# Optimization experiments

Hardware: AMD Instinct MI355X
Metric: run time of the kernel (lower is better)

The kernel has to match this reference:

```python
import jax, jax.numpy as jnp
import numpy as np

N = 50000          # nodes
E = 800000         # edges (avg degree 16)
IN_C = 3
HEADS = 4
NUM_GRAPHS = 8
NUM_CLASSES = 10


def setup_inputs() -> dict:
    key = jax.random.key(0)
    ks = jax.random.split(key, 12)
    x = jax.random.normal(ks[0], (N, IN_C), jnp.float32)
    edge_index = jax.random.randint(ks[1], (2, E), 0, N, dtype=jnp.int64)
    batch = jnp.sort(jax.random.randint(ks[2], (N,), 0, NUM_GRAPHS, dtype=jnp.int64))

    def glorot(k, shape, fan):
        return jax.random.normal(k, shape, jnp.float32) * np.float32(1.0 / np.sqrt(fan))

    return {
        "x": x, "edge_index": edge_index, "batch": batch,
        "fc0_w": glorot(ks[3], (IN_C, 16), IN_C), "fc0_b": jnp.zeros((16,), jnp.float32),
        "u1": glorot(ks[4], (16, HEADS), 16), "c1": jnp.zeros((HEADS,), jnp.float32),
        "w1": glorot(ks[5], (16, HEADS * 32), 16), "b1": jnp.zeros((32,), jnp.float32),
        "u2": glorot(ks[6], (32, HEADS), 32), "c2": jnp.zeros((HEADS,), jnp.float32),
        "w2": glorot(ks[7], (32, HEADS * 64), 32), "b2": jnp.zeros((64,), jnp.float32),
        "fc1_w": glorot(ks[8], (64, NUM_CLASSES), 64), "fc1_b": jnp.zeros((NUM_CLASSES,), jnp.float32),
    }


def feast_conv(x, src, dst, u, c, w, b, heads, out_c):
    """FeaStConv (t_inv=True): per-edge head softmax on (x_j - x_i), mean aggregation."""
    n = x.shape[0]
    # soft-assignment over heads: [E, H]
    q = jax.nn.softmax((x[src] - x[dst]) @ u + c, axis=-1)
    # transform at node level, then gather per edge: [E, H, out_c]
    xw = (x @ w).reshape(n, heads, out_c)
    msg = jnp.einsum('eh,ehc->ec', q, xw[src])           # [E, out_c]
    agg = jax.ops.segment_sum(msg, dst, num_segments=n)  # sum over incoming edges
    cnt = jax.ops.segment_sum(jnp.ones((src.shape[0],), x.dtype), dst, num_segments=n)
    return agg / jnp.maximum(cnt, 1.0)[:, None] + b


def global_mean_pool(x, batch, num_graphs):
    s = jax.ops.segment_sum(x, batch, num_segments=num_graphs)
    cnt = jax.ops.segment_sum(jnp.ones((x.shape[0],), x.dtype), batch, num_segments=num_graphs)
    return s / jnp.maximum(cnt, 1.0)[:, None]


def reference(x, edge_index, batch, fc0_w, fc0_b, u1, c1, w1, b1, u2, c2, w2, b2, fc1_w, fc1_b):
    src, dst = edge_index[0], edge_index[1]   # x_j = x[src], x_i = x[dst]
    h = jax.nn.relu(x @ fc0_w + fc0_b)                              # [N, 16]
    h = jax.nn.relu(feast_conv(h, src, dst, u1, c1, w1, b1, HEADS, 32))  # [N, 32]
    h = jax.nn.relu(feast_conv(h, src, dst, u2, c2, w2, b2, HEADS, 64))  # [N, 64]
    g = global_mean_pool(h, batch, NUM_GRAPHS)                      # [G, 64]
    # dropout is identity in eval mode
    return g @ fc1_w + fc1_b                                        # [G, num_classes]
```

## Files before the change

kernel.cpp:

```cpp
#include <hip/hip_runtime.h>

#define N_NODES 50000
#define N_EDGES 800000
#define HEADS 4
#define NUM_GRAPHS 8

__global__ __launch_bounds__(256) void hist_kernel(const int* __restrict__ dst,
                                                   int* __restrict__ deg,
                                                   int* __restrict__ off) {
  int e = blockIdx.x * blockDim.x + threadIdx.x;
  if (e < N_EDGES) off[e] = atomicAdd(&deg[dst[e]], 1);
}

__global__ __launch_bounds__(256) void alloc_kernel(const int* __restrict__ deg,
                                                    int* __restrict__ gctr,
                                                    int* __restrict__ rowstart) {
  int i = blockIdx.x * blockDim.x + threadIdx.x;
  int lane = threadIdx.x & 63;
  int d = (i < N_NODES) ? deg[i] : 0;
  int pre = d;
#pragma unroll
  for (int offd = 1; offd < 64; offd <<= 1) {
    int v = __shfl_up(pre, offd, 64);
    if (lane >= offd) pre += v;
  }
  int total = __shfl(pre, 63, 64);
  int base = 0;
  if (lane == 63) base = atomicAdd(gctr, total);
  base = __shfl(base, 63, 64);
  if (i < N_NODES) rowstart[i] = base + pre - d;
}

__global__ __launch_bounds__(256) void scatter_kernel(const int* __restrict__ src,
                                                      const int* __restrict__ dst,
                                                      const int* __restrict__ rowstart,
                                                      const int* __restrict__ off,
                                                      int2* __restrict__ sd) {
  int e = blockIdx.x * blockDim.x + threadIdx.x;
  if (e >= N_EDGES) return;
  int d = dst[e];
  int p = rowstart[d] + off[e];
  sd[p] = make_int2(src[e], d);
}

__global__ __launch_bounds__(256) void fc0_kernel(
    const float* __restrict__ x,
    const float* __restrict__ fc0_w, const float* __restrict__ fc0_b,
    const float* __restrict__ u1,
    float* __restrict__ h0, float* __restrict__ P1) {
  __shared__ float sW0[3 * 16];
  __shared__ float sB0[16];
  __shared__ float sU[16 * 4];
  for (int i = threadIdx.x; i < 48; i += blockDim.x) sW0[i] = fc0_w[i];
  for (int i = threadIdx.x; i < 16; i += blockDim.x) sB0[i] = fc0_b[i];
  for (int i = threadIdx.x; i < 64; i += blockDim.x) sU[i] = u1[i];
  __syncthreads();
  int n = blockIdx.x * blockDim.x + threadIdx.x;
  if (n >= N_NODES) return;
  float x0 = x[n * 3 + 0], x1 = x[n * 3 + 1], x2 = x[n * 3 + 2];
  float h[16];
#pragma unroll
  for (int j = 0; j < 16; j++) {
    float v = x0 * sW0[0 * 16 + j] + x1 * sW0[1 * 16 + j] + x2 * sW0[2 * 16 + j] + sB0[j];
    h[j] = fmaxf(v, 0.f);
    h0[(size_t)n * 16 + j] = h[j];
  }
  float p0 = 0.f, p1 = 0.f, p2 = 0.f, p3 = 0.f;
#pragma unroll
  for (int j = 0; j < 16; j++) {
    p0 += h[j] * sU[j * 4 + 0];
    p1 += h[j] * sU[j * 4 + 1];
    p2 += h[j] * sU[j * 4 + 2];
    p3 += h[j] * sU[j * 4 + 3];
  }
  reinterpret_cast<float4*>(P1)[n] = make_float4(p0, p1, p2, p3);
}

__global__ __launch_bounds__(256) void q_kernel(
    const int2* __restrict__ sd,
    const float* __restrict__ P, const float* __restrict__ cb,
    float* __restrict__ q_perm) {
  int p = blockIdx.x * blockDim.x + threadIdx.x;
  if (p >= N_EDGES) return;
  int2 e = sd[p];
  float4 Ps = reinterpret_cast<const float4*>(P)[e.x];
  float4 Pd = reinterpret_cast<const float4*>(P)[e.y];
  float l0 = Ps.x - Pd.x + cb[0];
  float l1 = Ps.y - Pd.y + cb[1];
  float l2 = Ps.z - Pd.z + cb[2];
  float l3 = Ps.w - Pd.w + cb[3];
  float m = fmaxf(fmaxf(l0, l1), fmaxf(l2, l3));
  float e0v = __expf(l0 - m), e1v = __expf(l1 - m), e2v = __expf(l2 - m), e3v = __expf(l3 - m);
  float inv = 1.f / (e0v + e1v + e2v + e3v);
  reinterpret_cast<float4*>(q_perm)[p] =
      make_float4(e0v * inv, e1v * inv, e2v * inv, e3v * inv);
}

__global__ __launch_bounds__(256) void agg1_kernel(
    const int* __restrict__ rowstart, const int* __restrict__ deg,
    const int2* __restrict__ sd, const float* __restrict__ q_perm,
    const float* __restrict__ h0,
    float* __restrict__ A) {
  int wave = threadIdx.x >> 6;
  int lane = threadIdx.x & 63;
  int g = lane >> 4;
  int j = lane & 15;
  int node = blockIdx.x * 4 + wave;
  if (node >= N_NODES) return;
  int e0 = rowstart[node];
  int e1 = e0 + deg[node];
  const float4* q4 = reinterpret_cast<const float4*>(q_perm);
  float a0 = 0.f, a1 = 0.f, a2 = 0.f, a3 = 0.f;
  int p = e0;
  for (; p + 16 <= e1; p += 16) {
    int sA = sd[p + 0 + g].x;
    int sB = sd[p + 4 + g].x;
    int sC = sd[p + 8 + g].x;
    int sD = sd[p + 12 + g].x;
    float4 qA = q4[p + 0 + g];
    float4 qB = q4[p + 4 + g];
    float4 qC = q4[p + 8 + g];
    float4 qD = q4[p + 12 + g];
    float fA = h0[(size_t)sA * 16 + j];
    float fB = h0[(size_t)sB * 16 + j];
    float fC = h0[(size_t)sC * 16 + j];
    float fD = h0[(size_t)sD * 16 + j];
    a0 += qA.x * fA + qB.x * fB + qC.x * fC + qD.x * fD;
    a1 += qA.y * fA + qB.y * fB + qC.y * fC + qD.y * fD;
    a2 += qA.z * fA + qB.z * fB + qC.z * fC + qD.z * fD;
    a3 += qA.w * fA + qB.w * fB + qC.w * fC + qD.w * fD;
  }
  for (; p + 4 <= e1; p += 4) {
    int s = sd[p + g].x;
    float4 q = q4[p + g];
    float f = h0[(size_t)s * 16 + j];
    a0 += q.x * f; a1 += q.y * f; a2 += q.z * f; a3 += q.w * f;
  }
  int rem = e1 - p;
  if (g < rem) {
    int s = sd[p + g].x;
    float4 q = q4[p + g];
    float f = h0[(size_t)s * 16 + j];
    a0 += q.x * f; a1 += q.y * f; a2 += q.z * f; a3 += q.w * f;
  }
  a0 += __shfl_xor(a0, 16, 64); a0 += __shfl_xor(a0, 32, 64);
  a1 += __shfl_xor(a1, 16, 64); a1 += __shfl_xor(a1, 32, 64);
  a2 += __shfl_xor(a2, 16, 64); a2 += __shfl_xor(a2, 32, 64);
  a3 += __shfl_xor(a3, 16, 64); a3 += __shfl_xor(a3, 32, 64);
  float o = (g == 0) ? a0 : (g == 1) ? a1 : (g == 2) ? a2 : a3;
  A[(size_t)node * 64 + lane] = o;
}

__global__ __launch_bounds__(256) void agg2_kernel(
    const int* __restrict__ rowstart, const int* __restrict__ deg,
    const int2* __restrict__ sd, const float* __restrict__ q_perm,
    const float* __restrict__ h1,
    float* __restrict__ A) {
  int wave = threadIdx.x >> 6;
  int lane = threadIdx.x & 63;
  int g = lane >> 5;
  int j = lane & 31;
  int node = blockIdx.x * 4 + wave;
  if (node >= N_NODES) return;
  int e0 = rowstart[node];
  int e1 = e0 + deg[node];
  const float4* q4 = reinterpret_cast<const float4*>(q_perm);
  float a0 = 0.f, a1 = 0.f, a2 = 0.f, a3 = 0.f;
  int p = e0;
  for (; p + 8 <= e1; p += 8) {
    int sA = sd[p + 0 + g].x;
    int sB = sd[p + 2 + g].x;
    int sC = sd[p + 4 + g].x;
    int sD = sd[p + 6 + g].x;
    float4 qA = q4[p + 0 + g];
    float4 qB = q4[p + 2 + g];
    float4 qC = q4[p + 4 + g];
    float4 qD = q4[p + 6 + g];
    float fA = h1[(size_t)sA * 32 + j];
    float fB = h1[(size_t)sB * 32 + j];
    float fC = h1[(size_t)sC * 32 + j];
    float fD = h1[(size_t)sD * 32 + j];
    a0 += qA.x * fA + qB.x * fB + qC.x * fC + qD.x * fD;
    a1 += qA.y * fA + qB.y * fB + qC.y * fC + qD.y * fD;
    a2 += qA.z * fA + qB.z * fB + qC.z * fC + qD.z * fD;
    a3 += qA.w * fA + qB.w * fB + qC.w * fC + qD.w * fD;
  }
  for (; p + 2 <= e1; p += 2) {
    int s = sd[p + g].x;
    float4 q = q4[p + g];
    float f = h1[(size_t)s * 32 + j];
    a0 += q.x * f; a1 += q.y * f; a2 += q.z * f; a3 += q.w * f;
  }
  int rem = e1 - p;
  if (g < rem) {
    int s = sd[p + g].x;
    float4 q = q4[p + g];
    float f = h1[(size_t)s * 32 + j];
    a0 += q.x * f; a1 += q.y * f; a2 += q.z * f; a3 += q.w * f;
  }
  a0 += __shfl_xor(a0, 32, 64);
  a1 += __shfl_xor(a1, 32, 64);
  a2 += __shfl_xor(a2, 32, 64);
  a3 += __shfl_xor(a3, 32, 64);
  float oa = (g == 0) ? a0 : a1;
  float ob = (g == 0) ? a2 : a3;
  A[(size_t)node * 128 + lane] = oa;
  A[(size_t)node * 128 + 64 + lane] = ob;
}

__global__ __launch_bounds__(256) void gemm1_kernel(
    const int* __restrict__ deg, const float* __restrict__ A,
    const float* __restrict__ w1, const float* __restrict__ b1,
    const float* __restrict__ u2,
    float* __restrict__ h1, float* __restrict__ P2) {
  __shared__ float sB[64 * 32];
  __shared__ float sU[32 * 4];
  for (int i = threadIdx.x; i < 64 * 32; i += 256) {
    int hj = i / 32, c = i % 32;
    sB[i] = w1[(hj % 16) * 128 + (hj / 16) * 32 + c];
  }
  for (int i = threadIdx.x; i < 128; i += 256) sU[i] = u2[i];
  __syncthreads();
  const float4* sB4 = reinterpret_cast<const float4*>(sB);
  int c4 = threadIdx.x & 7;
  int g = threadIdx.x >> 3;
  int n0 = blockIdx.x * 64 + g * 2;
  int n1 = n0 + 1;
  int na = min(n0, N_NODES - 1);
  int nb = min(n1, N_NODES - 1);
  const float4* A0 = reinterpret_cast<const float4*>(A + (size_t)na * 64);
  const float4* A1 = reinterpret_cast<const float4*>(A + (size_t)nb * 64);
  float4 bc = reinterpret_cast<const float4*>(b1)[c4];
  float4 acc0 = {0, 0, 0, 0}, acc1 = {0, 0, 0, 0};
#pragma unroll 2
  for (int k4 = 0; k4 < 16; k4++) {
    float4 a0 = A0[k4];
    float4 a1 = A1[k4];
    float4 w0 = sB4[(4 * k4 + 0) * 8 + c4];
    float4 wv1 = sB4[(4 * k4 + 1) * 8 + c4];
    float4 w2v = sB4[(4 * k4 + 2) * 8 + c4];
    float4 w3 = sB4[(4 * k4 + 3) * 8 + c4];
    acc0.x += a0.x * w0.x + a0.y * wv1.x + a0.z * w2v.x + a0.w * w3.x;
    acc0.y += a0.x * w0.y + a0.y * wv1.y + a0.z * w2v.y + a0.w * w3.y;
    acc0.z += a0.x * w0.z + a0.y * wv1.z + a0.z * w2v.z + a0.w * w3.z;
    acc0.w += a0.x * w0.w + a0.y * wv1.w + a0.z * w2v.w + a0.w * w3.w;
    acc1.x += a1.x * w0.x + a1.y * wv1.x + a1.z * w2v.x + a1.w * w3.x;
    acc1.y += a1.x * w0.y + a1.y * wv1.y + a1.z * w2v.y + a1.w * w3.y;
    acc1.z += a1.x * w0.z + a1.y * wv1.z + a1.z * w2v.z + a1.w * w3.z;
    acc1.w += a1.x * w0.w + a1.y * wv1.w + a1.z * w2v.w + a1.w * w3.w;
  }
  float inv0 = 1.f / fmaxf((float)deg[na], 1.f);
  float inv1 = 1.f / fmaxf((float)deg[nb], 1.f);
  float4 o0 = {fmaxf(acc0.x * inv0 + bc.x, 0.f), fmaxf(acc0.y * inv0 + bc.y, 0.f),
               fmaxf(acc0.z * inv0 + bc.z, 0.f), fmaxf(acc0.w * inv0 + bc.w, 0.f)};
  float4 o1 = {fmaxf(acc1.x * inv1 + bc.x, 0.f), fmaxf(acc1.y * inv1 + bc.y, 0.f),
               fmaxf(acc1.z * inv1 + bc.z, 0.f), fmaxf(acc1.w * inv1 + bc.w, 0.f)};
  if (n0 < N_NODES) reinterpret_cast<float4*>(h1 + (size_t)n0 * 32)[c4] = o0;
  if (n1 < N_NODES) reinterpret_cast<float4*>(h1 + (size_t)n1 * 32)[c4] = o1;
  float pa[4] = {0, 0, 0, 0}, pb[4] = {0, 0, 0, 0};
#pragma unroll
  for (int k = 0; k < 4; k++) {
    int c = 4 * c4 + k;
    float v0 = k == 0 ? o0.x : k == 1 ? o0.y : k == 2 ? o0.z : o0.w;
    float v1 = k == 0 ? o1.x : k == 1 ? o1.y : k == 2 ? o1.z : o1.w;
#pragma unroll
    for (int hh = 0; hh < 4; hh++) {
      pa[hh] += v0 * sU[c * 4 + hh];
      pb[hh] += v1 * sU[c * 4 + hh];
    }
  }
#pragma unroll
  for (int msk = 1; msk <= 4; msk <<= 1) {
#pragma unroll
    for (int hh = 0; hh < 4; hh++) {
      pa[hh] += __shfl_xor(pa[hh], msk, 64);
      pb[hh] += __shfl_xor(pb[hh], msk, 64);
    }
  }
  if (c4 == 0) {
    if (n0 < N_NODES)
      reinterpret_cast<float4*>(P2)[n0] = make_float4(pa[0], pa[1], pa[2], pa[3]);
    if (n1 < N_NODES)
      reinterpret_cast<float4*>(P2)[n1] = make_float4(pb[0], pb[1], pb[2], pb[3]);
  }
}

__global__ __launch_bounds__(256) void gemm2_kernel(
    const int* __restrict__ deg, const float* __restrict__ A,
    const float* __restrict__ w2, const float* __restrict__ b2,
    float* __restrict__ h2) {
  __shared__ float sB[128 * 64];
  for (int i = threadIdx.x; i < 128 * 64; i += 256) {
    int hj = i / 64, c = i % 64;
    sB[i] = w2[(hj % 32) * 256 + (hj / 32) * 64 + c];
  }
  __syncthreads();
  const float4* sB4 = reinterpret_cast<const float4*>(sB);
  int c4 = threadIdx.x & 15;
  int g = threadIdx.x >> 4;
  int n0 = blockIdx.x * 32 + g * 2;
  int n1 = n0 + 1;
  int na = min(n0, N_NODES - 1);
  int nb = min(n1, N_NODES - 1);
  const float4* A0 = reinterpret_cast<const float4*>(A + (size_t)na * 128);
  const float4* A1 = reinterpret_cast<const float4*>(A + (size_t)nb * 128);
  float4 bc = reinterpret_cast<const float4*>(b2)[c4];
  float4 acc0 = {0, 0, 0, 0}, acc1 = {0, 0, 0, 0};
#pragma unroll 2
  for (int k4 = 0; k4 < 32; k4++) {
    float4 a0 = A0[k4];
    float4 a1 = A1[k4];
    float4 w0 = sB4[(4 * k4 + 0) * 16 + c4];
    float4 wv1 = sB4[(4 * k4 + 1) * 16 + c4];
    float4 w2v = sB4[(4 * k4 + 2) * 16 + c4];
    float4 w3 = sB4[(4 * k4 + 3) * 16 + c4];
    acc0.x += a0.x * w0.x + a0.y * wv1.x + a0.z * w2v.x + a0.w * w3.x;
    acc0.y += a0.x * w0.y + a0.y * wv1.y + a0.z * w2v.y + a0.w * w3.y;
    acc0.z += a0.x * w0.z + a0.y * wv1.z + a0.z * w2v.z + a0.w * w3.z;
    acc0.w += a0.x * w0.w + a0.y * wv1.w + a0.z * w2v.w + a0.w * w3.w;
    acc1.x += a1.x * w0.x + a1.y * wv1.x + a1.z * w2v.x + a1.w * w3.x;
    acc1.y += a1.x * w0.y + a1.y * wv1.y + a1.z * w2v.y + a1.w * w3.y;
    acc1.z += a1.x * w0.z + a1.y * wv1.z + a1.z * w2v.z + a1.w * w3.z;
    acc1.w += a1.x * w0.w + a1.y * wv1.w + a1.z * w2v.w + a1.w * w3.w;
  }
  if (n0 < N_NODES) {
    float inv = 1.f / fmaxf((float)deg[n0], 1.f);
    float4 o = {fmaxf(acc0.x * inv + bc.x, 0.f), fmaxf(acc0.y * inv + bc.y, 0.f),
                fmaxf(acc0.z * inv + bc.z, 0.f), fmaxf(acc0.w * inv + bc.w, 0.f)};
    reinterpret_cast<float4*>(h2 + (size_t)n0 * 64)[c4] = o;
  }
  if (n1 < N_NODES) {
    float inv = 1.f / fmaxf((float)deg[n1], 1.f);
    float4 o = {fmaxf(acc1.x * inv + bc.x, 0.f), fmaxf(acc1.y * inv + bc.y, 0.f),
                fmaxf(acc1.z * inv + bc.z, 0.f), fmaxf(acc1.w * inv + bc.w, 0.f)};
    reinterpret_cast<float4*>(h2 + (size_t)n1 * 64)[c4] = o;
  }
}

#define POOL_CHUNK 64
__global__ __launch_bounds__(256) void pool_kernel(
    const float* __restrict__ h2, const int* __restrict__ batch,
    float* __restrict__ gsum, float* __restrict__ gcnt) {
  int grp = threadIdx.x / 64;
  int c = threadIdx.x % 64;
  int n0 = (blockIdx.x * 4 + grp) * POOL_CHUNK;
  int n1 = min(n0 + POOL_CHUNK, N_NODES);
  if (n0 >= N_NODES) return;
  float acc = 0.f;
  float cacc = 0.f;
  int curg = batch[n0];
  for (int n = n0; n < n1; n++) {
    int g = batch[n];
    float v = h2[(size_t)n * 64 + c];
    if (g != curg) {
      atomicAdd(&gsum[curg * 64 + c], acc);
      if (c == 0) atomicAdd(&gcnt[curg], cacc);
      acc = 0.f;
      cacc = 0.f;
      curg = g;
    }
    acc += v;
    cacc += 1.f;
  }
  atomicAdd(&gsum[curg * 64 + c], acc);
  if (c == 0) atomicAdd(&gcnt[curg], cacc);
}

__global__ __launch_bounds__(128) void head_kernel(
    const float* __restrict__ gsum, const float* __restrict__ gcnt,
    const float* __restrict__ fc1_w, const float* __restrict__ fc1_b,
    float* __restrict__ out) {
  int t = threadIdx.x;
  if (t >= NUM_GRAPHS * 10) return;
  int g = t / 10, k = t % 10;
  float inv = 1.f / fmaxf(gcnt[g], 1.f);
  float s = fc1_b[k];
#pragma unroll
  for (int c = 0; c < 64; c++) s += gsum[g * 64 + c] * inv * fc1_w[c * 10 + k];
  out[g * 10 + k] = s;
}

extern "C" void kernel_launch(void* const* d_in, const int* in_sizes, int n_in,
                              void* d_out, int out_size, void* d_ws, size_t ws_size,
                              hipStream_t stream) {
  const float* x = (const float*)d_in[0];
  const int* edge_index = (const int*)d_in[1];
  const int* batch = (const int*)d_in[2];
  const float* fc0_w = (const float*)d_in[3];
  const float* fc0_b = (const float*)d_in[4];
  const float* u1 = (const float*)d_in[5];
  const float* c1 = (const float*)d_in[6];
  const float* w1 = (const float*)d_in[7];
  const float* b1 = (const float*)d_in[8];
  const float* u2 = (const float*)d_in[9];
  const float* c2 = (const float*)d_in[10];
  const float* w2 = (const float*)d_in[11];
  const float* b2 = (const float*)d_in[12];
  const float* fc1_w = (const float*)d_in[13];
  const float* fc1_b = (const float*)d_in[14];
  float* out = (float*)d_out;

  const int* src = edge_index;
  const int* dst = edge_index + N_EDGES;

  char* wsb = (char*)d_ws;
  int* deg = (int*)wsb;
  int* gctr = deg + N_NODES;
  float* gsum = (float*)wsb + 50004;
  float* gcnt = gsum + NUM_GRAPHS * 64;
  int* rowstart = (int*)wsb + 50524;
  int* off = rowstart + N_NODES;
  int2* sd = (int2*)((int*)wsb + 900524);
  float* q_perm = (float*)wsb + 2500524;
  float* h0 = q_perm + (size_t)N_EDGES * 4;
  float* h1 = h0 + (size_t)N_NODES * 16;
  float* h2 = h1 + (size_t)N_NODES * 32;
  float* A = h2 + (size_t)N_NODES * 64;
  float* P1 = A + (size_t)N_NODES * 128;
  float* P2 = P1 + (size_t)N_NODES * 4;

  hipMemsetAsync(d_ws, 0, 50524 * sizeof(int), stream);

  int nblk = (N_NODES + 255) / 256;
  int eblk = (N_EDGES + 255) / 256;
  int wblk = (N_NODES + 3) / 4;

  hist_kernel<<<eblk, 256, 0, stream>>>(dst, deg, off);
  alloc_kernel<<<nblk, 256, 0, stream>>>(deg, gctr, rowstart);
  scatter_kernel<<<eblk, 256, 0, stream>>>(src, dst, rowstart, off, sd);

  fc0_kernel<<<nblk, 256, 0, stream>>>(x, fc0_w, fc0_b, u1, h0, P1);

  q_kernel<<<eblk, 256, 0, stream>>>(sd, P1, c1, q_perm);
  agg1_kernel<<<wblk, 256, 0, stream>>>(rowstart, deg, sd, q_perm, h0, A);
  gemm1_kernel<<<(N_NODES + 63) / 64, 256, 0, stream>>>(deg, A, w1, b1, u2, h1, P2);

  q_kernel<<<eblk, 256, 0, stream>>>(sd, P2, c2, q_perm);
  agg2_kernel<<<wblk, 256, 0, stream>>>(rowstart, deg, sd, q_perm, h1, A);
  gemm2_kernel<<<(N_NODES + 31) / 32, 256, 0, stream>>>(deg, A, w2, b2, h2);

  int pblk = (N_NODES + POOL_CHUNK * 4 - 1) / (POOL_CHUNK * 4);
  pool_kernel<<<pblk, 256, 0, stream>>>(h2, batch, gsum, gcnt);
  head_kernel<<<1, 128, 0, stream>>>(gsum, gcnt, fc1_w, fc1_b, out);
}
```

Measured before the change: 281.7 us.

## Fuse edge softmax into aggregation kernels and merge histogram with fc0

After: 275.3 us, median of 3. 1.02x faster.

```diff
diff --git a/kernel.cpp b/kernel.cpp
--- a/kernel.cpp
+++ b/kernel.cpp
@@ -5,11 +5,46 @@
 #define HEADS 4
 #define NUM_GRAPHS 8
 
-__global__ __launch_bounds__(256) void hist_kernel(const int* __restrict__ dst,
-                                                   int* __restrict__ deg,
-                                                   int* __restrict__ off) {
-  int e = blockIdx.x * blockDim.x + threadIdx.x;
-  if (e < N_EDGES) off[e] = atomicAdd(&deg[dst[e]], 1);
+#define EBLK ((N_EDGES + 255) / 256)
+#define NBLK ((N_NODES + 255) / 256)
+
+__global__ __launch_bounds__(256) void hist_fc0_kernel(
+    const int* __restrict__ dst, int* __restrict__ deg, int* __restrict__ off,
+    const float* __restrict__ x,
+    const float* __restrict__ fc0_w, const float* __restrict__ fc0_b,
+    const float* __restrict__ u1,
+    float* __restrict__ h0, float* __restrict__ P1) {
+  if (blockIdx.x < EBLK) {
+    int e = blockIdx.x * 256 + threadIdx.x;
+    if (e < N_EDGES) off[e] = atomicAdd(&deg[dst[e]], 1);
+    return;
+  }
+  __shared__ float sW0[3 * 16];
+  __shared__ float sB0[16];
+  __shared__ float sU[16 * 4];
+  for (int i = threadIdx.x; i < 48; i += 256) sW0[i] = fc0_w[i];
+  for (int i = threadIdx.x; i < 16; i += 256) sB0[i] = fc0_b[i];
+  for (int i = threadIdx.x; i < 64; i += 256) sU[i] = u1[i];
+  __syncthreads();
+  int n = (blockIdx.x - EBLK) * 256 + threadIdx.x;
+  if (n >= N_NODES) return;
+  float x0 = x[n * 3 + 0], x1 = x[n * 3 + 1], x2 = x[n * 3 + 2];
+  float h[16];
+#pragma unroll
+  for (int j = 0; j < 16; j++) {
+    float v = x0 * sW0[0 * 16 + j] + x1 * sW0[1 * 16 + j] + x2 * sW0[2 * 16 + j] + sB0[j];
+    h[j] = fmaxf(v, 0.f);
+    h0[(size_t)n * 16 + j] = h[j];
+  }
+  float p0 = 0.f, p1 = 0.f, p2 = 0.f, p3 = 0.f;
+#pragma unroll
+  for (int j = 0; j < 16; j++) {
+    p0 += h[j] * sU[j * 4 + 0];
+    p1 += h[j] * sU[j * 4 + 1];
+    p2 += h[j] * sU[j * 4 + 2];
+    p3 += h[j] * sU[j * 4 + 3];
+  }
+  reinterpret_cast<float4*>(P1)[n] = make_float4(p0, p1, p2, p3);
 }
 
 __global__ __launch_bounds__(256) void alloc_kernel(const int* __restrict__ deg,
@@ -35,70 +70,24 @@
                                                       const int* __restrict__ dst,
                                                       const int* __restrict__ rowstart,
                                                       const int* __restrict__ off,
-                                                      int2* __restrict__ sd) {
+                                                      int* __restrict__ src_perm) {
   int e = blockIdx.x * blockDim.x + threadIdx.x;
   if (e >= N_EDGES) return;
-  int d = dst[e];
-  int p = rowstart[d] + off[e];
-  sd[p] = make_int2(src[e], d);
-}
-
-__global__ __launch_bounds__(256) void fc0_kernel(
-    const float* __restrict__ x,
-    const float* __restrict__ fc0_w, const float* __restrict__ fc0_b,
-    const float* __restrict__ u1,
-    float* __restrict__ h0, float* __restrict__ P1) {
-  __shared__ float sW0[3 * 16];
-  __shared__ float sB0[16];
-  __shared__ float sU[16 * 4];
-  for (int i = threadIdx.x; i < 48; i += blockDim.x) sW0[i] = fc0_w[i];
-  for (int i = threadIdx.x; i < 16; i += blockDim.x) sB0[i] = fc0_b[i];
-  for (int i = threadIdx.x; i < 64; i += blockDim.x) sU[i] = u1[i];
-  __syncthreads();
-  int n = blockIdx.x * blockDim.x + threadIdx.x;
-  if (n >= N_NODES) return;
-  float x0 = x[n * 3 + 0], x1 = x[n * 3 + 1], x2 = x[n * 3 + 2];
-  float h[16];
-#pragma unroll
-  for (int j = 0; j < 16; j++) {
-    float v = x0 * sW0[0 * 16 + j] + x1 * sW0[1 * 16 + j] + x2 * sW0[2 * 16 + j] + sB0[j];
-    h[j] = fmaxf(v, 0.f);
-    h0[(size_t)n * 16 + j] = h[j];
-  }
-  float p0 = 0.f, p1 = 0.f, p2 = 0.f, p3 = 0.f;
-#pragma unroll
-  for (int j = 0; j < 16; j++) {
-    p0 += h[j] * sU[j * 4 + 0];
-    p1 += h[j] * sU[j * 4 + 1];
-    p2 += h[j] * sU[j * 4 + 2];
-    p3 += h[j] * sU[j * 4 + 3];
-  }
-  reinterpret_cast<float4*>(P1)[n] = make_float4(p0, p1, p2, p3);
-}
-
-__global__ __launch_bounds__(256) void q_kernel(
-    const int2* __restrict__ sd,
-    const float* __restrict__ P, const float* __restrict__ cb,
-    float* __restrict__ q_perm) {
-  int p = blockIdx.x * blockDim.x + threadIdx.x;
-  if (p >= N_EDGES) return;
-  int2 e = sd[p];
-  float4 Ps = reinterpret_cast<const float4*>(P)[e.x];
-  float4 Pd = reinterpret_cast<const float4*>(P)[e.y];
-  float l0 = Ps.x - Pd.x + cb[0];
-  float l1 = Ps.y - Pd.y + cb[1];
-  float l2 = Ps.z - Pd.z + cb[2];
-  float l3 = Ps.w - Pd.w + cb[3];
+  src_perm[rowstart[dst[e]] + off[e]] = src[e];
+}
+
+__device__ __forceinline__ float4 edge_q(float4 Ps, float b0, float b1, float b2, float b3) {
+  float l0 = Ps.x + b0, l1 = Ps.y + b1, l2 = Ps.z + b2, l3 = Ps.w + b3;
   float m = fmaxf(fmaxf(l0, l1), fmaxf(l2, l3));
-  float e0v = __expf(l0 - m), e1v = __expf(l1 - m), e2v = __expf(l2 - m), e3v = __expf(l3 - m);
-  float inv = 1.f / (e0v + e1v + e2v + e3v);
-  reinterpret_cast<float4*>(q_perm)[p] =
-      make_float4(e0v * inv, e1v * inv, e2v * inv, e3v * inv);
+  float e0 = __expf(l0 - m), e1 = __expf(l1 - m), e2 = __expf(l2 - m), e3 = __expf(l3 - m);
+  float inv = 1.f / (e0 + e1 + e2 + e3);
+  return make_float4(e0 * inv, e1 * inv, e2 * inv, e3 * inv);
 }
 
 __global__ __launch_bounds__(256) void agg1_kernel(
     const int* __restrict__ rowstart, const int* __restrict__ deg,
-    const int2* __restrict__ sd, const float* __restrict__ q_perm,
+    const int* __restrict__ src_perm,
+    const float* __restrict__ P1, const float* __restrict__ c1,
     const float* __restrict__ h0,
     float* __restrict__ A) {
   int wave = threadIdx.x >> 6;
@@ -107,40 +96,48 @@
   int j = lane & 15;
   int node = blockIdx.x * 4 + wave;
   if (node >= N_NODES) return;
+  float4 Pd = reinterpret_cast<const float4*>(P1)[node];
+  float b0 = c1[0] - Pd.x, b1 = c1[1] - Pd.y, b2 = c1[2] - Pd.z, b3 = c1[3] - Pd.w;
   int e0 = rowstart[node];
   int e1 = e0 + deg[node];
-  const float4* q4 = reinterpret_cast<const float4*>(q_perm);
+  const float4* P4 = reinterpret_cast<const float4*>(P1);
   float a0 = 0.f, a1 = 0.f, a2 = 0.f, a3 = 0.f;
   int p = e0;
   for (; p + 16 <= e1; p += 16) {
-    int sA = sd[p + 0 + g].x;
-    int sB = sd[p + 4 + g].x;
-    int sC = sd[p + 8 + g].x;
-    int sD = sd[p + 12 + g].x;
-    float4 qA = q4[p + 0 + g];
-    float4 qB = q4[p + 4 + g];
-    float4 qC = q4[p + 8 + g];
-    float4 qD = q4[p + 12 + g];
+    int sA = src_perm[p + 0 + g];
+    int sB = src_perm[p + 4 + g];
+    int sC = src_perm[p + 8 + g];
+    int sD = src_perm[p + 12 + g];
+    float4 PA = P4[sA];
+    float4 PB = P4[sB];
+    float4 PC = P4[sC];
+    float4 PD = P4[sD];
     float fA = h0[(size_t)sA * 16 + j];
     float fB = h0[(size_t)sB * 16 + j];
     float fC = h0[(size_t)sC * 16 + j];
     float fD = h0[(size_t)sD * 16 + j];
+    float4 qA = edge_q(PA, b0, b1, b2, b3);
+    float4 qB = edge_q(PB, b0, b1, b2, b3);
+    float4 qC = edge_q(PC, b0, b1, b2, b3);
+    float4 qD = edge_q(PD, b0, b1, b2, b3);
     a0 += qA.x * fA + qB.x * fB + qC.x * fC + qD.x * fD;
     a1 += qA.y * fA + qB.y * fB + qC.y * fC + qD.y * fD;
     a2 += qA.z * fA + qB.z * fB + qC.z * fC + qD.z * fD;
     a3 += qA.w * fA + qB.w * fB + qC.w * fC + qD.w * fD;
   }
   for (; p + 4 <= e1; p += 4) {
-    int s = sd[p + g].x;
-    float4 q = q4[p + g];
+    int s = src_perm[p + g];
+    float4 Ps = P4[s];
     float f = h0[(size_t)s * 16 + j];
+    float4 q = edge_q(Ps, b0, b1, b2, b3);
     a0 += q.x * f; a1 += q.y * f; a2 += q.z * f; a3 += q.w * f;
   }
   int rem = e1 - p;
   if (g < rem) {
-    int s = sd[p + g].x;
-    float4 q = q4[p + g];
+    int s = src_perm[p + g];
+    float4 Ps = P4[s];
     float f = h0[(size_t)s * 16 + j];
+    float4 q = edge_q(Ps, b0, b1, b2, b3);
     a0 += q.x * f; a1 += q.y * f; a2 += q.z * f; a3 += q.w * f;
   }
   a0 += __shfl_xor(a0, 16, 64); a0 += __shfl_xor(a0, 32, 64);
@@ -153,7 +150,8 @@
 
 __global__ __launch_bounds__(256) void agg2_kernel(
     const int* __restrict__ rowstart, const int* __restrict__ deg,
-    const int2* __restrict__ sd, const float* __restrict__ q_perm,
+    const int* __restrict__ src_perm,
+    const float* __restrict__ P2, const float* __restrict__ c2,
     const float* __restrict__ h1,
     float* __restrict__ A) {
   int wave = threadIdx.x >> 6;
@@ -162,40 +160,48 @@
   int j = lane & 31;
   int node = blockIdx.x * 4 + wave;
   if (node >= N_NODES) return;
+  float4 Pd = reinterpret_cast<const float4*>(P2)[node];
+  float b0 = c2[0] - Pd.x, b1 = c2[1] - Pd.y, b2 = c2[2] - Pd.z, b3 = c2[3] - Pd.w;
   int e0 = rowstart[node];
   int e1 = e0 + deg[node];
-  const float4* q4 = reinterpret_cast<const float4*>(q_perm);
+  const float4* P4 = reinterpret_cast<const float4*>(P2);
   float a0 = 0.f, a1 = 0.f, a2 = 0.f, a3 = 0.f;
   int p = e0;
   for (; p + 8 <= e1; p += 8) {
-    int sA = sd[p + 0 + g].x;
-    int sB = sd[p + 2 + g].x;
-    int sC = sd[p + 4 + g].x;
-    int sD = sd[p + 6 + g].x;
-    float4 qA = q4[p + 0 + g];
-    float4 qB = q4[p + 2 + g];
-    float4 qC = q4[p + 4 + g];
-    float4 qD = q4[p + 6 + g];
+    int sA = src_perm[p + 0 + g];
+    int sB = src_perm[p + 2 + g];
+    int sC = src_perm[p + 4 + g];
+    int sD = src_perm[p + 6 + g];
+    float4 PA = P4[sA];
+    float4 PB = P4[sB];
+    float4 PC = P4[sC];
+    float4 PD = P4[sD];
     float fA = h1[(size_t)sA * 32 + j];
     float fB = h1[(size_t)sB * 32 + j];
     float fC = h1[(size_t)sC * 32 + j];
     float fD = h1[(size_t)sD * 32 + j];
+    float4 qA = edge_q(PA, b0, b1, b2, b3);
+    float4 qB = edge_q(PB, b0, b1, b2, b3);
+    float4 qC = edge_q(PC, b0, b1, b2, b3);
+    float4 qD = edge_q(PD, b0, b1, b2, b3);
     a0 += qA.x * fA + qB.x * fB + qC.x * fC + qD.x * fD;
     a1 += qA.y * fA + qB.y * fB + qC.y * fC + qD.y * fD;
     a2 += qA.z * fA + qB.z * fB + qC.z * fC + qD.z * fD;
     a3 += qA.w * fA + qB.w * fB + qC.w * fC + qD.w * fD;
   }
   for (; p + 2 <= e1; p += 2) {
-    int s = sd[p + g].x;
-    float4 q = q4[p + g];
+    int s = src_perm[p + g];
+    float4 Ps = P4[s];
     float f = h1[(size_t)s * 32 + j];
+    float4 q = edge_q(Ps, b0, b1, b2, b3);
     a0 += q.x * f; a1 += q.y * f; a2 += q.z * f; a3 += q.w * f;
   }
   int rem = e1 - p;
   if (g < rem) {
-    int s = sd[p + g].x;
-    float4 q = q4[p + g];
+    int s = src_perm[p + g];
+    float4 Ps = P4[s];
     float f = h1[(size_t)s * 32 + j];
+    float4 q = edge_q(Ps, b0, b1, b2, b3);
     a0 += q.x * f; a1 += q.y * f; a2 += q.z * f; a3 += q.w * f;
   }
   a0 += __shfl_xor(a0, 32, 64);
@@ -410,9 +416,8 @@
   float* gcnt = gsum + NUM_GRAPHS * 64;
   int* rowstart = (int*)wsb + 50524;
   int* off = rowstart + N_NODES;
-  int2* sd = (int2*)((int*)wsb + 900524);
-  float* q_perm = (float*)wsb + 2500524;
-  float* h0 = q_perm + (size_t)N_EDGES * 4;
+  int* src_perm = off + N_EDGES;
+  float* h0 = (float*)wsb + 1700524;
   float* h1 = h0 + (size_t)N_NODES * 16;
   float* h2 = h1 + (size_t)N_NODES * 32;
   float* A = h2 + (size_t)N_NODES * 64;
@@ -421,22 +426,18 @@
 
   hipMemsetAsync(d_ws, 0, 50524 * sizeof(int), stream);
 
-  int nblk = (N_NODES + 255) / 256;
-  int eblk = (N_EDGES + 255) / 256;
+  int nblk = NBLK;
+  int eblk = EBLK;
   int wblk = (N_NODES + 3) / 4;
 
-  hist_kernel<<<eblk, 256, 0, stream>>>(dst, deg, off);
+  hist_fc0_kernel<<<eblk + nblk, 256, 0, stream>>>(dst, deg, off, x, fc0_w, fc0_b, u1, h0, P1);
   alloc_kernel<<<nblk, 256, 0, stream>>>(deg, gctr, rowstart);
-  scatter_kernel<<<eblk, 256, 0, stream>>>(src, dst, rowstart, off, sd);
-
-  fc0_kernel<<<nblk, 256, 0, stream>>>(x, fc0_w, fc0_b, u1, h0, P1);
-
-  q_kernel<<<eblk, 256, 0, stream>>>(sd, P1, c1, q_perm);
-  agg1_kernel<<<wblk, 256, 0, stream>>>(rowstart, deg, sd, q_perm, h0, A);
+  scatter_kernel<<<eblk, 256, 0, stream>>>(src, dst, rowstart, off, src_perm);
+
+  agg1_kernel<<<wblk, 256, 0, stream>>>(rowstart, deg, src_perm, P1, c1, h0, A);
   gemm1_kernel<<<(N_NODES + 63) / 64, 256, 0, stream>>>(deg, A, w1, b1, u2, h1, P2);
 
-  q_kernel<<<eblk, 256, 0, stream>>>(sd, P2, c2, q_perm);
-  agg2_kernel<<<wblk, 256, 0, stream>>>(rowstart, deg, sd, q_perm, h1, A);
+  agg2_kernel<<<wblk, 256, 0, stream>>>(rowstart, deg, src_perm, P2, c2, h1, A);
   gemm2_kernel<<<(N_NODES + 31) / 32, 256, 0, stream>>>(deg, A, w2, b2, h2);
 
   int pblk = (N_NODES + POOL_CHUNK * 4 - 1) / (POOL_CHUNK * 4);
```
